# Performance work log

Measured on AMD Instinct MI355X. Metric: run time of the kernel, lower is better.

Reference implementation:

```python
import jax, jax.numpy as jnp
import numpy as np

HIDDEN = 768
NUM_HEADS = 12
HEAD_DIM = HIDDEN // NUM_HEADS


def setup_inputs() -> dict:
    key = jax.random.key(0)
    ks = jax.random.split(key, 10)
    B, S = 4, 2048
    scale = 1.0 / np.sqrt(HIDDEN)
    inp = {
        "hidden_states": jax.random.normal(ks[0], (B, S, HIDDEN), dtype=jnp.float32),
        "attention_mask": jnp.ones((B, S), dtype=jnp.float32),
        "Wq": jax.random.normal(ks[1], (HIDDEN, HIDDEN), dtype=jnp.float32) * scale,
        "bq": jnp.zeros((HIDDEN,), dtype=jnp.float32),
        "Wk": jax.random.normal(ks[2], (HIDDEN, HIDDEN), dtype=jnp.float32) * scale,
        "bk": jnp.zeros((HIDDEN,), dtype=jnp.float32),
        "Wv": jax.random.normal(ks[3], (HIDDEN, HIDDEN), dtype=jnp.float32) * scale,
        "bv": jnp.zeros((HIDDEN,), dtype=jnp.float32),
        "Wo": jax.random.normal(ks[4], (HIDDEN, HIDDEN), dtype=jnp.float32) * scale,
        "bo": jnp.zeros((HIDDEN,), dtype=jnp.float32),
    }
    return inp


def _split_heads(x):
    # [B,S,H] -> [B,nh,S,dh]
    B, S, _ = x.shape
    return x.reshape(B, S, NUM_HEADS, HEAD_DIM).transpose(0, 2, 1, 3)


def reference(hidden_states, attention_mask, Wq, bq, Wk, bk, Wv, bv, Wo, bo):
    # Linear projections (torch nn.Linear: x @ W.T + b; here W stored as [in,out])
    q = _split_heads(hidden_states @ Wq + bq)
    k = _split_heads(hidden_states @ Wk + bk)
    v = _split_heads(hidden_states @ Wv + bv)

    # scores: [B,nh,S,S]
    scores = jnp.einsum("bhqd,bhkd->bhqk", q, k) / np.sqrt(HEAD_DIM).astype(np.float32)

    # outer-product mask: [B,1,S,S], broadcast over heads
    ext = (attention_mask[:, :, None] * attention_mask[:, None, :])[:, None, :, :]
    scores = ext * scores - (1.0 - ext) * 1e9

    probs = jax.nn.softmax(scores, axis=-1)
    ctx = jnp.einsum("bhqk,bhkd->bhqd", probs, v)  # [B,nh,S,dh]
    B, _, S, _ = ctx.shape
    ctx = ctx.transpose(0, 2, 1, 3).reshape(B, S, HIDDEN)
    out = ctx @ Wo + bo
    # torch F.gelu default: exact (erf-based)
    return jax.nn.gelu(out, approximate=False)
```

## Files before the change

### kernel.cpp

```cpp
#include <hip/hip_runtime.h>
#include <math.h>

#define HIDDEN 768
#define NH 12
#define DH 64
#define SEQ 2048
#define BATCH 4

typedef __bf16 bf16;
typedef bf16 bf16x4 __attribute__((ext_vector_type(4)));
typedef bf16 bf16x8 __attribute__((ext_vector_type(8)));
typedef float f32x4 __attribute__((ext_vector_type(4)));

__global__ __launch_bounds__(256) void prep_x(const float* __restrict__ X,
                                              bf16* __restrict__ Xb) {
    const size_t i = ((size_t)blockIdx.x * 256 + threadIdx.x) * 8;
    float4 a = *(const float4*)(X + i);
    float4 b = *(const float4*)(X + i + 4);
    bf16x8 o = {(bf16)a.x, (bf16)a.y, (bf16)a.z, (bf16)a.w,
                (bf16)b.x, (bf16)b.y, (bf16)b.z, (bf16)b.w};
    *(bf16x8*)(Xb + i) = o;
}

__global__ __launch_bounds__(256) void prep_w(const float* __restrict__ Wq,
                                              const float* __restrict__ Wk,
                                              const float* __restrict__ Wv,
                                              const float* __restrict__ Wo,
                                              bf16* __restrict__ Wt,
                                              bf16* __restrict__ Wot_hi,
                                              bf16* __restrict__ Wot_lo) {
    __shared__ float Ts[64][68];
    const int tid = threadIdx.x;
    const int n0 = blockIdx.x * 64, k0 = blockIdx.y * 64, z = blockIdx.z;
    const float* W = (z == 0) ? Wq : (z == 1) ? Wk : (z == 2) ? Wv : Wo;

    {
        const int r = tid >> 2, c = (tid & 3) << 4;
        const float* src = W + (size_t)(k0 + r) * HIDDEN + n0 + c;
#pragma unroll
        for (int j = 0; j < 4; ++j)
            *(float4*)&Ts[r][c + 4 * j] = *(const float4*)(src + 4 * j);
    }
    __syncthreads();

    const int nl = tid >> 2, kc = (tid & 3) << 4;
    float v[16];
#pragma unroll
    for (int j = 0; j < 16; ++j) v[j] = Ts[kc + j][nl];

    if (z < 3) {
        bf16 hi[16];
#pragma unroll
        for (int j = 0; j < 16; ++j) hi[j] = (bf16)v[j];
        const size_t off = (size_t)(z * HIDDEN + n0 + nl) * HIDDEN + k0 + kc;
        *(bf16x8*)(Wt + off) = *(bf16x8*)&hi[0];
        *(bf16x8*)(Wt + off + 8) = *(bf16x8*)&hi[8];
    } else {
        bf16 hi[16], lo[16];
#pragma unroll
        for (int j = 0; j < 16; ++j) {
            hi[j] = (bf16)v[j];
            lo[j] = (bf16)(v[j] - (float)hi[j]);
        }
        const size_t off = (size_t)(n0 + nl) * HIDDEN + k0 + kc;
        *(bf16x8*)(Wot_hi + off) = *(bf16x8*)&hi[0];
        *(bf16x8*)(Wot_hi + off + 8) = *(bf16x8*)&hi[8];
        *(bf16x8*)(Wot_lo + off) = *(bf16x8*)&lo[0];
        *(bf16x8*)(Wot_lo + off + 8) = *(bf16x8*)&lo[8];
    }
}

__global__ __launch_bounds__(256) void gemm_qkv(
    const bf16* __restrict__ Xb, const bf16* __restrict__ Wt,
    const float* __restrict__ bq, const float* __restrict__ bk,
    const float* __restrict__ bv, bf16* __restrict__ q_out,
    bf16* __restrict__ k_out, bf16* __restrict__ v_out) {
    __shared__ bf16 As[128][40];
    __shared__ bf16 Bs[128][40];

    const int tid = threadIdx.x;
    const int ln = tid & 63, wv = tid >> 6;
    const int quad = ln >> 4, l16 = ln & 15;
    const int wm = wv >> 1, wn = wv & 1;
    const int n0 = blockIdx.x * 128, m0 = blockIdx.y * 128;

    f32x4 acc[4][4];
#pragma unroll
    for (int i = 0; i < 4; ++i)
#pragma unroll
        for (int j = 0; j < 4; ++j) acc[i][j] = (f32x4){0.f, 0.f, 0.f, 0.f};

    const int sr = tid >> 1, sc = (tid & 1) << 4;
    const bf16* gA = Xb + (size_t)(m0 + sr) * HIDDEN + sc;
    const bf16* gB = Wt + (size_t)(n0 + sr) * HIDDEN + sc;

    bf16x8 ar0, ar1, br0, br1;
    ar0 = *(const bf16x8*)gA;
    ar1 = *(const bf16x8*)(gA + 8);
    br0 = *(const bf16x8*)gB;
    br1 = *(const bf16x8*)(gB + 8);

    for (int k0 = 0; k0 < HIDDEN; k0 += 32) {
        __syncthreads();
        *(bf16x8*)&As[sr][sc] = ar0;
        *(bf16x8*)&As[sr][sc + 8] = ar1;
        *(bf16x8*)&Bs[sr][sc] = br0;
        *(bf16x8*)&Bs[sr][sc + 8] = br1;
        __syncthreads();
        if (k0 + 32 < HIDDEN) {
            ar0 = *(const bf16x8*)(gA + k0 + 32);
            ar1 = *(const bf16x8*)(gA + k0 + 40);
            br0 = *(const bf16x8*)(gB + k0 + 32);
            br1 = *(const bf16x8*)(gB + k0 + 40);
        }

        bf16x8 ah[4], bh[4];
#pragma unroll
        for (int i = 0; i < 4; ++i) {
            ah[i] = *(bf16x8*)&As[wm * 64 + i * 16 + l16][quad * 8];
            bh[i] = *(bf16x8*)&Bs[wn * 64 + i * 16 + l16][quad * 8];
        }
#pragma unroll
        for (int mi = 0; mi < 4; ++mi)
#pragma unroll
            for (int ni = 0; ni < 4; ++ni)
                acc[mi][ni] = __builtin_amdgcn_mfma_f32_16x16x32_bf16(
                    ah[mi], bh[ni], acc[mi][ni], 0, 0, 0);
    }

    const int nb = n0 + wn * 64;
    const int which = nb / HIDDEN;
    const int nrel = nb - which * HIDDEN;
    const int h = nrel >> 6;

    if (which < 2) {
        const float scale = (which == 0) ? 0.18033688011112042f : 1.0f;
        const float* bias = (which == 0) ? bq : bk;
        bf16* dst = (which == 0) ? q_out : k_out;
#pragma unroll
        for (int ni = 0; ni < 4; ++ni) {
            const int dh = ni * 16 + l16;
            const float bb = bias[nrel + dh];
#pragma unroll
            for (int mi = 0; mi < 4; ++mi)
#pragma unroll
                for (int r = 0; r < 4; ++r) {
                    const int m = m0 + wm * 64 + mi * 16 + quad * 4 + r;
                    const int bi = m >> 11, s = m & (SEQ - 1);
                    dst[(((size_t)(bi * NH + h) * SEQ + s) << 6) + dh] =
                        (bf16)(scale * (acc[mi][ni][r] + bb));
                }
        }
    } else {
        const int bi = m0 >> 11;
        const int sbase = (m0 & (SEQ - 1)) + wm * 64;
#pragma unroll
        for (int ni = 0; ni < 4; ++ni) {
            const int dh = ni * 16 + l16;
            const float bb = bv[nrel + dh];
            bf16* vrow = v_out + ((size_t)(bi * NH + h) * DH + dh) * SEQ;
#pragma unroll
            for (int mi = 0; mi < 4; ++mi) {
                bf16x4 pk = {(bf16)(acc[mi][ni][0] + bb),
                             (bf16)(acc[mi][ni][1] + bb),
                             (bf16)(acc[mi][ni][2] + bb),
                             (bf16)(acc[mi][ni][3] + bb)};
                *(bf16x4*)(vrow + sbase + mi * 16 + quad * 4) = pk;
            }
        }
    }
}

__global__ __launch_bounds__(256) void attn_mfma(const bf16* __restrict__ Q,
                                                 const bf16* __restrict__ K,
                                                 const bf16* __restrict__ Vt,
                                                 const float* __restrict__ mask,
                                                 float* __restrict__ ctx) {
    __shared__ bf16 Ks[64 * 64];
    __shared__ bf16 Vts[64 * 64];
    __shared__ bf16 Ps[128 * 64];
    __shared__ float Ms[SEQ];
    __shared__ int allones_s;

    const int tid = threadIdx.x;
    const int ln = tid & 63, w = tid >> 6;
    const int quad = ln >> 4, l16 = ln & 15;
    const int qt = blockIdx.x, h = blockIdx.y, b = blockIdx.z;
    const size_t bh = (size_t)b * NH + h;
    const bf16* Qp = Q + ((bh * SEQ + (size_t)qt * 128) << 6);
    const bf16* Kp = K + (bh * SEQ << 6);
    const bf16* Vp = Vt + (bh * DH) * SEQ;

    if (tid == 0) allones_s = 1;
    {
        float4 m0 = *(const float4*)(mask + (size_t)b * SEQ + tid * 8);
        float4 m1 = *(const float4*)(mask + (size_t)b * SEQ + tid * 8 + 4);
        *(float4*)&Ms[tid * 8] = m0;
        *(float4*)&Ms[tid * 8 + 4] = m1;
        bool ok = (m0.x == 1.f) & (m0.y == 1.f) & (m0.z == 1.f) &
                  (m0.w == 1.f) & (m1.x == 1.f) & (m1.y == 1.f) &
                  (m1.z == 1.f) & (m1.w == 1.f);
        __syncthreads();
        if (!ok) allones_s = 0;
    }
    __syncthreads();
    const bool fastmask = (allones_s != 0);

    bf16x8 qb[2][2];
#pragma unroll
    for (int qg = 0; qg < 2; ++qg)
#pragma unroll
        for (int hf = 0; hf < 2; ++hf)
            qb[qg][hf] = *(const bf16x8*)(Qp + ((w * 32 + qg * 16 + l16) << 6) +
                                          hf * 32 + quad * 8);
    float mq[2];
#pragma unroll
    for (int qg = 0; qg < 2; ++qg)
        mq[qg] = Ms[qt * 128 + w * 32 + qg * 16 + l16];

    float l_i[2] = {0.f, 0.f};
    f32x4 acc[4][2];
#pragma unroll
    for (int fd = 0; fd < 4; ++fd)
#pragma unroll
        for (int qg = 0; qg < 2; ++qg) acc[fd][qg] = (f32x4){0.f, 0.f, 0.f, 0.f};

    const int sr = tid >> 2, sc = (tid & 3) << 4;
    const int ssw = (sr & 7) << 3;
    const int d0 = sc ^ ssw, d1 = (sc + 8) ^ ssw;
    const bf16* kbase = Kp + ((size_t)sr << 6) + sc;
    const bf16* vbase = Vp + (size_t)sr * SEQ + sc;

    bf16x8 kr0, kr1, vr0, vr1;
    kr0 = *(const bf16x8*)kbase;
    kr1 = *(const bf16x8*)(kbase + 8);
    vr0 = *(const bf16x8*)vbase;
    vr1 = *(const bf16x8*)(vbase + 8);

    for (int kt = 0; kt < SEQ / 64; ++kt) {
        __syncthreads();
        *(bf16x8*)&Ks[sr * 64 + d0] = kr0;
        *(bf16x8*)&Ks[sr * 64 + d1] = kr1;
        *(bf16x8*)&Vts[sr * 64 + d0] = vr0;
        *(bf16x8*)&Vts[sr * 64 + d1] = vr1;
        __syncthreads();
        if (kt + 1 < SEQ / 64) {
            kr0 = *(const bf16x8*)(kbase + ((size_t)(kt + 1) << 12));
            kr1 = *(const bf16x8*)(kbase + ((size_t)(kt + 1) << 12) + 8);
            vr0 = *(const bf16x8*)(vbase + (kt + 1) * 64);
            vr1 = *(const bf16x8*)(vbase + (kt + 1) * 64 + 8);
        }

        const int fsw = (l16 & 7) << 3;
        f32x4 st[4][2];
#pragma unroll
        for (int f = 0; f < 4; ++f) {
            const int krow = (f * 16 + l16) * 64;
            bf16x8 ka0 = *(bf16x8*)&Ks[krow + ((quad * 8) ^ fsw)];
            bf16x8 ka1 = *(bf16x8*)&Ks[krow + ((32 + quad * 8) ^ fsw)];
#pragma unroll
            for (int qg = 0; qg < 2; ++qg) {
                f32x4 c = {0.f, 0.f, 0.f, 0.f};
                c = __builtin_amdgcn_mfma_f32_16x16x32_bf16(ka0, qb[qg][0], c, 0, 0, 0);
                c = __builtin_amdgcn_mfma_f32_16x16x32_bf16(ka1, qb[qg][1], c, 0, 0, 0);
                st[f][qg] = c;
            }
        }

        if (!fastmask) {
#pragma unroll
            for (int f = 0; f < 4; ++f) {
                const float4 mk4 = *(const float4*)&Ms[kt * 64 + f * 16 + quad * 4];
                const float mkk[4] = {mk4.x, mk4.y, mk4.z, mk4.w};
#pragma unroll
                for (int qg = 0; qg < 2; ++qg)
#pragma unroll
                    for (int r = 0; r < 4; ++r) {
                        const float ext = mq[qg] * mkk[r];
                        st[f][qg][r] =
                            ext * st[f][qg][r] - (1.0f - ext) * 1.4426950e9f;
                    }
            }
        }

#pragma unroll
        for (int qg = 0; qg < 2; ++qg) {
            const int row = w * 32 + qg * 16 + l16;
            const int sw = (row & 7) << 3;
            bf16* prow = &Ps[row * 64];
#pragma unroll
            for (int f = 0; f < 4; ++f) {
                float p0 = __builtin_amdgcn_exp2f(st[f][qg][0]);
                float p1 = __builtin_amdgcn_exp2f(st[f][qg][1]);
                float p2 = __builtin_amdgcn_exp2f(st[f][qg][2]);
                float p3 = __builtin_amdgcn_exp2f(st[f][qg][3]);
                l_i[qg] += (p0 + p1) + (p2 + p3);
                bf16x4 pk = {(bf16)p0, (bf16)p1, (bf16)p2, (bf16)p3};
                *(bf16x4*)&prow[(f * 16 + quad * 4) ^ sw] = pk;
            }
        }

        bf16x8 pb[2][2];
#pragma unroll
        for (int qg = 0; qg < 2; ++qg) {
            const int row = w * 32 + qg * 16 + l16;
            const int sw = (row & 7) << 3;
#pragma unroll
            for (int hf = 0; hf < 2; ++hf)
                pb[qg][hf] =
                    *(bf16x8*)&Ps[row * 64 + ((hf * 32 + quad * 8) ^ sw)];
        }
#pragma unroll
        for (int fd = 0; fd < 4; ++fd) {
            const int vrow = (fd * 16 + l16) * 64;
            bf16x8 va0 = *(bf16x8*)&Vts[vrow + ((quad * 8) ^ fsw)];
            bf16x8 va1 = *(bf16x8*)&Vts[vrow + ((32 + quad * 8) ^ fsw)];
#pragma unroll
            for (int qg = 0; qg < 2; ++qg) {
                f32x4 c = acc[fd][qg];
                c = __builtin_amdgcn_mfma_f32_16x16x32_bf16(va0, pb[qg][0], c, 0, 0, 0);
                c = __builtin_amdgcn_mfma_f32_16x16x32_bf16(va1, pb[qg][1], c, 0, 0, 0);
                acc[fd][qg] = c;
            }
        }
    }

#pragma unroll
    for (int qg = 0; qg < 2; ++qg) {
        l_i[qg] += __shfl_xor(l_i[qg], 16);
        l_i[qg] += __shfl_xor(l_i[qg], 32);
    }

#pragma unroll
    for (int qg = 0; qg < 2; ++qg) {
        const float inv = 1.0f / l_i[qg];
        const size_t row = (size_t)b * SEQ + qt * 128 + w * 32 + qg * 16 + l16;
#pragma unroll
        for (int fd = 0; fd < 4; ++fd) {
            float4 o = {acc[fd][qg][0] * inv, acc[fd][qg][1] * inv,
                        acc[fd][qg][2] * inv, acc[fd][qg][3] * inv};
            *(float4*)(ctx + row * HIDDEN + h * 64 + fd * 16 + quad * 4) = o;
        }
    }
}

__global__ __launch_bounds__(256) void gemm_out(const float* __restrict__ ctx,
                                                const bf16* __restrict__ Bhi,
                                                const bf16* __restrict__ Blo,
                                                const float* __restrict__ bo,
                                                float* __restrict__ fout) {
    __shared__ bf16 As_hi[128][40];
    __shared__ bf16 As_lo[128][40];
    __shared__ bf16 Bs_hi[64][40];
    __shared__ bf16 Bs_lo[64][40];

    const int tid = threadIdx.x;
    const int ln = tid & 63, wv = tid >> 6;
    const int quad = ln >> 4, l16 = ln & 15;
    const int wm = wv >> 1, wn = wv & 1;
    const int n0 = blockIdx.x * 64, m0 = blockIdx.y * 128;

    f32x4 acc[4][2];
#pragma unroll
    for (int i = 0; i < 4; ++i)
#pragma unroll
        for (int j = 0; j < 2; ++j) acc[i][j] = (f32x4){0.f, 0.f, 0.f, 0.f};

    const int sra = tid >> 1, sca = (tid & 1) << 4;
    const int srb = tid >> 2, scb = (tid & 3) << 3;
    const float* gA = ctx + (size_t)(m0 + sra) * HIDDEN + sca;
    const bf16* gBh = Bhi + (size_t)(n0 + srb) * HIDDEN + scb;
    const bf16* gBl = Blo + (size_t)(n0 + srb) * HIDDEN + scb;

    float fa[16];
    bf16x8 brh, brl;
#pragma unroll
    for (int j = 0; j < 4; ++j) *(float4*)&fa[4 * j] = *(const float4*)(gA + 4 * j);
    brh = *(const bf16x8*)gBh;
    brl = *(const bf16x8*)gBl;

    for (int k0 = 0; k0 < HIDDEN; k0 += 32) {
        bf16 hi[16], lo[16];
#pragma unroll
        for (int j = 0; j < 16; ++j) {
            hi[j] = (bf16)fa[j];
            lo[j] = (bf16)(fa[j] - (float)hi[j]);
        }
        __syncthreads();
        *(bf16x8*)&As_hi[sra][sca] = *(bf16x8*)&hi[0];
        *(bf16x8*)&As_hi[sra][sca + 8] = *(bf16x8*)&hi[8];
        *(bf16x8*)&As_lo[sra][sca] = *(bf16x8*)&lo[0];
        *(bf16x8*)&As_lo[sra][sca + 8] = *(bf16x8*)&lo[8];
        *(bf16x8*)&Bs_hi[srb][scb] = brh;
        *(bf16x8*)&Bs_lo[srb][scb] = brl;
        __syncthreads();
        if (k0 + 32 < HIDDEN) {
#pragma unroll
            for (int j = 0; j < 4; ++j)
                *(float4*)&fa[4 * j] = *(const float4*)(gA + k0 + 32 + 4 * j);
            brh = *(const bf16x8*)(gBh + k0 + 32);
            brl = *(const bf16x8*)(gBl + k0 + 32);
        }

        bf16x8 ah[4], al[4], bh[2], bl[2];
#pragma unroll
        for (int i = 0; i < 4; ++i) {
            ah[i] = *(bf16x8*)&As_hi[wm * 64 + i * 16 + l16][quad * 8];
            al[i] = *(bf16x8*)&As_lo[wm * 64 + i * 16 + l16][quad * 8];
        }
#pragma unroll
        for (int i = 0; i < 2; ++i) {
            bh[i] = *(bf16x8*)&Bs_hi[wn * 32 + i * 16 + l16][quad * 8];
            bl[i] = *(bf16x8*)&Bs_lo[wn * 32 + i * 16 + l16][quad * 8];
        }
#pragma unroll
        for (int mi = 0; mi < 4; ++mi)
#pragma unroll
            for (int ni = 0; ni < 2; ++ni) {
                f32x4 c = acc[mi][ni];
                c = __builtin_amdgcn_mfma_f32_16x16x32_bf16(ah[mi], bh[ni], c, 0, 0, 0);
                c = __builtin_amdgcn_mfma_f32_16x16x32_bf16(ah[mi], bl[ni], c, 0, 0, 0);
                c = __builtin_amdgcn_mfma_f32_16x16x32_bf16(al[mi], bh[ni], c, 0, 0, 0);
                acc[mi][ni] = c;
            }
    }

#pragma unroll
    for (int ni = 0; ni < 2; ++ni) {
        const int n = n0 + wn * 32 + ni * 16 + l16;
        const float bb = bo[n];
#pragma unroll
        for (int mi = 0; mi < 4; ++mi)
#pragma unroll
            for (int r = 0; r < 4; ++r) {
                const int m = m0 + wm * 64 + mi * 16 + quad * 4 + r;
                float x = acc[mi][ni][r] + bb;
                x = 0.5f * x * (1.0f + erff(x * 0.70710678118654752440f));
                fout[(size_t)m * HIDDEN + n] = x;
            }
    }
}

extern "C" void kernel_launch(void* const* d_in, const int* in_sizes, int n_in,
                              void* d_out, int out_size, void* d_ws, size_t ws_size,
                              hipStream_t stream) {
    const float* X    = (const float*)d_in[0];
    const float* mask = (const float*)d_in[1];
    const float* Wq   = (const float*)d_in[2];
    const float* bq   = (const float*)d_in[3];
    const float* Wk   = (const float*)d_in[4];
    const float* bk   = (const float*)d_in[5];
    const float* Wv   = (const float*)d_in[6];
    const float* bv   = (const float*)d_in[7];
    const float* Wo   = (const float*)d_in[8];
    const float* bo   = (const float*)d_in[9];
    float* out = (float*)d_out;

    char* w = (char*)d_ws;
    const size_t NE = (size_t)BATCH * SEQ * HIDDEN;
    bf16* q_ws   = (bf16*)w;  w += NE * 2;
    bf16* k_ws   = (bf16*)w;  w += NE * 2;
    bf16* vt_ws  = (bf16*)w;  w += NE * 2;
    float* ctx   = (float*)w; w += NE * 4;
    bf16* Xb     = (bf16*)w;  w += NE * 2;
    bf16* Wt     = (bf16*)w;  w += (size_t)3 * HIDDEN * HIDDEN * 2;
    bf16* Wot_hi = (bf16*)w;  w += (size_t)HIDDEN * HIDDEN * 2;
    bf16* Wot_lo = (bf16*)w;  w += (size_t)HIDDEN * HIDDEN * 2;

    prep_x<<<(int)(NE / 2048), 256, 0, stream>>>(X, Xb);
    prep_w<<<dim3(12, 12, 4), 256, 0, stream>>>(Wq, Wk, Wv, Wo, Wt, Wot_hi,
                                                Wot_lo);
    gemm_qkv<<<dim3(18, 64), 256, 0, stream>>>(Xb, Wt, bq, bk, bv, q_ws, k_ws,
                                               vt_ws);
    attn_mfma<<<dim3(SEQ / 128, NH, BATCH), 256, 0, stream>>>(q_ws, k_ws, vt_ws,
                                                              mask, ctx);
    gemm_out<<<dim3(12, 64), 256, 0, stream>>>(ctx, Wot_hi, Wot_lo, bo, out);
}
```

Before: 270.8 us.

## Emit bf16 hi/lo context from attention, drop mask LDS, add MFMA priority

The attention kernel now splits its normalized output into bf16 hi and lo parts and writes those directly, so the output GEMM loads ready bf16 operands instead of converting fp32 context in its inner loop. The 8 KB shared mask buffer is removed and mask values are read from global memory, which lowers LDS use and may raise occupancy. s_setprio is raised around both MFMA blocks to favor waves issuing matrix instructions. Global traffic for the context stays the same size, and the split is now computed once per element instead of once per output tile that reads it.

Result: slower. 290.3 us (+7.2%).

```diff
diff --git a/kernel.cpp b/kernel.cpp
--- a/kernel.cpp
+++ b/kernel.cpp
@@ -175,11 +175,11 @@
                                                  const bf16* __restrict__ K,
                                                  const bf16* __restrict__ Vt,
                                                  const float* __restrict__ mask,
-                                                 float* __restrict__ ctx) {
+                                                 bf16* __restrict__ ctx_hi,
+                                                 bf16* __restrict__ ctx_lo) {
     __shared__ bf16 Ks[64 * 64];
     __shared__ bf16 Vts[64 * 64];
     __shared__ bf16 Ps[128 * 64];
-    __shared__ float Ms[SEQ];
     __shared__ int allones_s;
 
     const int tid = threadIdx.x;
@@ -190,13 +190,12 @@
     const bf16* Qp = Q + ((bh * SEQ + (size_t)qt * 128) << 6);
     const bf16* Kp = K + (bh * SEQ << 6);
     const bf16* Vp = Vt + (bh * DH) * SEQ;
+    const float* mrow = mask + (size_t)b * SEQ;
 
     if (tid == 0) allones_s = 1;
     {
-        float4 m0 = *(const float4*)(mask + (size_t)b * SEQ + tid * 8);
-        float4 m1 = *(const float4*)(mask + (size_t)b * SEQ + tid * 8 + 4);
-        *(float4*)&Ms[tid * 8] = m0;
-        *(float4*)&Ms[tid * 8 + 4] = m1;
+        float4 m0 = *(const float4*)(mrow + tid * 8);
+        float4 m1 = *(const float4*)(mrow + tid * 8 + 4);
         bool ok = (m0.x == 1.f) & (m0.y == 1.f) & (m0.z == 1.f) &
                   (m0.w == 1.f) & (m1.x == 1.f) & (m1.y == 1.f) &
                   (m1.z == 1.f) & (m1.w == 1.f);
@@ -216,7 +215,7 @@
     float mq[2];
 #pragma unroll
     for (int qg = 0; qg < 2; ++qg)
-        mq[qg] = Ms[qt * 128 + w * 32 + qg * 16 + l16];
+        mq[qg] = mrow[qt * 128 + w * 32 + qg * 16 + l16];
 
     float l_i[2] = {0.f, 0.f};
     f32x4 acc[4][2];
@@ -253,6 +252,7 @@
 
         const int fsw = (l16 & 7) << 3;
         f32x4 st[4][2];
+        __builtin_amdgcn_s_setprio(1);
 #pragma unroll
         for (int f = 0; f < 4; ++f) {
             const int krow = (f * 16 + l16) * 64;
@@ -266,11 +266,13 @@
                 st[f][qg] = c;
             }
         }
+        __builtin_amdgcn_s_setprio(0);
 
         if (!fastmask) {
 #pragma unroll
             for (int f = 0; f < 4; ++f) {
-                const float4 mk4 = *(const float4*)&Ms[kt * 64 + f * 16 + quad * 4];
+                const float4 mk4 =
+                    *(const float4*)(mrow + kt * 64 + f * 16 + quad * 4);
                 const float mkk[4] = {mk4.x, mk4.y, mk4.z, mk4.w};
 #pragma unroll
                 for (int qg = 0; qg < 2; ++qg)
@@ -310,6 +312,7 @@
                 pb[qg][hf] =
                     *(bf16x8*)&Ps[row * 64 + ((hf * 32 + quad * 8) ^ sw)];
         }
+        __builtin_amdgcn_s_setprio(1);
 #pragma unroll
         for (int fd = 0; fd < 4; ++fd) {
             const int vrow = (fd * 16 + l16) * 64;
@@ -323,6 +326,7 @@
                 acc[fd][qg] = c;
             }
         }
+        __builtin_amdgcn_s_setprio(0);
     }
 
 #pragma unroll
@@ -337,14 +341,22 @@
         const size_t row = (size_t)b * SEQ + qt * 128 + w * 32 + qg * 16 + l16;
 #pragma unroll
         for (int fd = 0; fd < 4; ++fd) {
-            float4 o = {acc[fd][qg][0] * inv, acc[fd][qg][1] * inv,
-                        acc[fd][qg][2] * inv, acc[fd][qg][3] * inv};
-            *(float4*)(ctx + row * HIDDEN + h * 64 + fd * 16 + quad * 4) = o;
-        }
-    }
-}
-
-__global__ __launch_bounds__(256) void gemm_out(const float* __restrict__ ctx,
+            bf16 hi[4], lo[4];
+#pragma unroll
+            for (int r = 0; r < 4; ++r) {
+                const float o = acc[fd][qg][r] * inv;
+                hi[r] = (bf16)o;
+                lo[r] = (bf16)(o - (float)hi[r]);
+            }
+            const size_t off = row * HIDDEN + h * 64 + fd * 16 + quad * 4;
+            *(bf16x4*)(ctx_hi + off) = *(bf16x4*)&hi[0];
+            *(bf16x4*)(ctx_lo + off) = *(bf16x4*)&lo[0];
+        }
+    }
+}
+
+__global__ __launch_bounds__(256) void gemm_out(const bf16* __restrict__ Ah,
+                                                const bf16* __restrict__ Al,
                                                 const bf16* __restrict__ Bhi,
                                                 const bf16* __restrict__ Blo,
                                                 const float* __restrict__ bo,
@@ -368,36 +380,33 @@
 
     const int sra = tid >> 1, sca = (tid & 1) << 4;
     const int srb = tid >> 2, scb = (tid & 3) << 3;
-    const float* gA = ctx + (size_t)(m0 + sra) * HIDDEN + sca;
+    const bf16* gAh = Ah + (size_t)(m0 + sra) * HIDDEN + sca;
+    const bf16* gAl = Al + (size_t)(m0 + sra) * HIDDEN + sca;
     const bf16* gBh = Bhi + (size_t)(n0 + srb) * HIDDEN + scb;
     const bf16* gBl = Blo + (size_t)(n0 + srb) * HIDDEN + scb;
 
-    float fa[16];
-    bf16x8 brh, brl;
-#pragma unroll
-    for (int j = 0; j < 4; ++j) *(float4*)&fa[4 * j] = *(const float4*)(gA + 4 * j);
+    bf16x8 arh0, arh1, arl0, arl1, brh, brl;
+    arh0 = *(const bf16x8*)gAh;
+    arh1 = *(const bf16x8*)(gAh + 8);
+    arl0 = *(const bf16x8*)gAl;
+    arl1 = *(const bf16x8*)(gAl + 8);
     brh = *(const bf16x8*)gBh;
     brl = *(const bf16x8*)gBl;
 
     for (int k0 = 0; k0 < HIDDEN; k0 += 32) {
-        bf16 hi[16], lo[16];
-#pragma unroll
-        for (int j = 0; j < 16; ++j) {
-            hi[j] = (bf16)fa[j];
-            lo[j] = (bf16)(fa[j] - (float)hi[j]);
-        }
-        __syncthreads();
-        *(bf16x8*)&As_hi[sra][sca] = *(bf16x8*)&hi[0];
-        *(bf16x8*)&As_hi[sra][sca + 8] = *(bf16x8*)&hi[8];
-        *(bf16x8*)&As_lo[sra][sca] = *(bf16x8*)&lo[0];
-        *(bf16x8*)&As_lo[sra][sca + 8] = *(bf16x8*)&lo[8];
+        __syncthreads();
+        *(bf16x8*)&As_hi[sra][sca] = arh0;
+        *(bf16x8*)&As_hi[sra][sca + 8] = arh1;
+        *(bf16x8*)&As_lo[sra][sca] = arl0;
+        *(bf16x8*)&As_lo[sra][sca + 8] = arl1;
         *(bf16x8*)&Bs_hi[srb][scb] = brh;
         *(bf16x8*)&Bs_lo[srb][scb] = brl;
         __syncthreads();
         if (k0 + 32 < HIDDEN) {
-#pragma unroll
-            for (int j = 0; j < 4; ++j)
-                *(float4*)&fa[4 * j] = *(const float4*)(gA + k0 + 32 + 4 * j);
+            arh0 = *(const bf16x8*)(gAh + k0 + 32);
+            arh1 = *(const bf16x8*)(gAh + k0 + 40);
+            arl0 = *(const bf16x8*)(gAl + k0 + 32);
+            arl1 = *(const bf16x8*)(gAl + k0 + 40);
             brh = *(const bf16x8*)(gBh + k0 + 32);
             brl = *(const bf16x8*)(gBl + k0 + 32);
         }
@@ -461,7 +470,8 @@
     bf16* q_ws   = (bf16*)w;  w += NE * 2;
     bf16* k_ws   = (bf16*)w;  w += NE * 2;
     bf16* vt_ws  = (bf16*)w;  w += NE * 2;
-    float* ctx   = (float*)w; w += NE * 4;
+    bf16* ctx_hi = (bf16*)w;  w += NE * 2;
+    bf16* ctx_lo = (bf16*)w;  w += NE * 2;
     bf16* Xb     = (bf16*)w;  w += NE * 2;
     bf16* Wt     = (bf16*)w;  w += (size_t)3 * HIDDEN * HIDDEN * 2;
     bf16* Wot_hi = (bf16*)w;  w += (size_t)HIDDEN * HIDDEN * 2;
@@ -472,7 +482,8 @@
                                                 Wot_lo);
     gemm_qkv<<<dim3(18, 64), 256, 0, stream>>>(Xb, Wt, bq, bk, bv, q_ws, k_ws,
                                                vt_ws);
-    attn_mfma<<<dim3(SEQ / 128, NH, BATCH), 256, 0, stream>>>(q_ws, k_ws, vt_ws,
-                                                              mask, ctx);
-    gemm_out<<<dim3(12, 64), 256, 0, stream>>>(ctx, Wot_hi, Wot_lo, bo, out);
-}
+    attn_mfma<<<dim3(SEQ / 128, NH, BATCH), 256, 0, stream>>>(
+        q_ws, k_ws, vt_ws, mask, ctx_hi, ctx_lo);
+    gemm_out<<<dim3(12, 64), 256, 0, stream>>>(ctx_hi, ctx_lo, Wot_hi, Wot_lo,
+                                               bo, out);
+}
```
